# Performance work log

Hardware: AMD Instinct MI355X
Metric: run time of the kernel (lower is better)

## Reference

```python
import jax, jax.numpy as jnp
import numpy as np

N, H = 8192, 1024

def setup_inputs() -> dict:
    key = jax.random.key(0)
    ks = jax.random.split(key, 7)
    s = 1.0 / np.sqrt(H)
    return {
        "x": jax.random.normal(ks[0], (N, H), dtype=jnp.float32),
        "Wq": jax.random.uniform(ks[1], (H, H), dtype=jnp.float32, minval=-s, maxval=s),
        "bq": jax.random.uniform(ks[2], (H,), dtype=jnp.float32, minval=-s, maxval=s),
        "Wk": jax.random.uniform(ks[3], (H, H), dtype=jnp.float32, minval=-s, maxval=s),
        "bk": jax.random.uniform(ks[4], (H,), dtype=jnp.float32, minval=-s, maxval=s),
        "Wv": jax.random.uniform(ks[5], (H, H), dtype=jnp.float32, minval=-s, maxval=s),
        "bv": jax.random.uniform(ks[6], (H,), dtype=jnp.float32, minval=-s, maxval=s),
    }

def reference(x, Wq, bq, Wk, bk, Wv, bv):
    # q/k/v projections: [N, H]
    q = x @ Wq + bq
    k = x @ Wk + bk
    v = x @ Wv + bv
    # full scores [N, N]; NOTE: original has no 1/sqrt(d) scaling
    scores = q @ k.T
    alpha = jax.nn.softmax(scores, axis=1)
    return alpha @ v
```

## Files before the change

kernel.cpp:

```cpp
#include <hip/hip_runtime.h>
#include <hip/hip_bf16.h>
#include <hip/hip_fp16.h>


typedef _Float16 f16x8 __attribute__((ext_vector_type(8)));
typedef _Float16 f16x2 __attribute__((ext_vector_type(2)));
typedef float floatx4 __attribute__((ext_vector_type(4)));
typedef float floatx2 __attribute__((ext_vector_type(2)));

__device__ __forceinline__ unsigned short f2h(float f) {
  __half h = __float2half(f);
  return __builtin_bit_cast(unsigned short, h);
}
__device__ __forceinline__ float h2f(unsigned short u) {
  return __half2float(__builtin_bit_cast(__half, u));
}

__device__ __forceinline__ float fdot2(unsigned a, unsigned b, float c) {
#if __has_builtin(__builtin_amdgcn_fdot2)
  return __builtin_amdgcn_fdot2(__builtin_bit_cast(f16x2, a),
                                __builtin_bit_cast(f16x2, b), c, false);
#else
  f16x2 av = __builtin_bit_cast(f16x2, a);
  f16x2 bv = __builtin_bit_cast(f16x2, b);
  return c + (float)av[0] * (float)bv[0] + (float)av[1] * (float)bv[1];
#endif
}

__device__ __forceinline__ void async16(const void* g, void* l) {
  __builtin_amdgcn_global_load_lds(
      (__attribute__((address_space(1))) unsigned int*)(g),
      (__attribute__((address_space(3))) unsigned int*)(l),
      16, 0, 0);
}


__global__ __launch_bounds__(256) void conv_f32_f16(const float* __restrict__ in,
                                                    unsigned short* __restrict__ out,
                                                    long n) {
  long i = ((long)blockIdx.x * 256 + threadIdx.x) * 4;
  if (i + 3 < n) {
    float4 f = *(const float4*)(in + i);
    ushort4 o;
    o.x = f2h(f.x); o.y = f2h(f.y); o.z = f2h(f.z); o.w = f2h(f.w);
    *(ushort4*)(out + i) = o;
  }
}

__global__ __launch_bounds__(256) void transpose_f32_f16_3(const float* __restrict__ in0,
                                                           const float* __restrict__ in1,
                                                           const float* __restrict__ in2,
                                                           unsigned short* __restrict__ out,
                                                           int rows, int cols) {
  const float* in = (blockIdx.z == 0) ? in0 : (blockIdx.z == 1) ? in1 : in2;
  unsigned short* o = out + (size_t)blockIdx.z * rows * cols;
  __shared__ float tile[32][33];
  int bx = blockIdx.x * 32;
  int by = blockIdx.y * 32;
  int tx = threadIdx.x & 31, ty = threadIdx.x >> 5;
  #pragma unroll
  for (int yy = ty; yy < 32; yy += 8)
    tile[yy][tx] = in[(size_t)(by + yy) * cols + bx + tx];
  __syncthreads();
  #pragma unroll
  for (int yy = ty; yy < 32; yy += 8)
    o[(size_t)(bx + yy) * rows + by + tx] = f2h(tile[tx][yy]);
}

template <int MODE>
__global__ __launch_bounds__(256, 4)
void gemm_bt(const unsigned short* __restrict__ A,
             const unsigned short* __restrict__ B,
             int M, int Nn, int K,
             const float* __restrict__ b0, const float* __restrict__ b1,
             const float* __restrict__ b2,
             unsigned short* __restrict__ out) {
  if constexpr (MODE == 0) {
    B   += (size_t)blockIdx.z * Nn * K;
    out += (size_t)blockIdx.z * M * Nn;
  }
  const float* bias = (MODE != 0) ? nullptr
                      : (blockIdx.z == 0) ? b0 : (blockIdx.z == 1) ? b1 : b2;

  unsigned bx = blockIdx.x, by = blockIdx.y;
  if constexpr (MODE == 1) {
    const unsigned nb  = gridDim.x * gridDim.y;
    const unsigned lin = blockIdx.y * gridDim.x + blockIdx.x;
    const unsigned swz = (lin & 7u) * (nb >> 3) + (lin >> 3);
    bx = swz % gridDim.x;
    by = swz / gridDim.x;
  }

  __shared__ unsigned short As[128 * 32];
  __shared__ unsigned short Bs[128 * 32];
  const int tid  = threadIdx.x;
  const int wave = tid >> 6;
  const int lane = tid & 63;
  const int wm = wave >> 1, wn = wave & 1;
  const int quad = lane >> 4, l16 = lane & 15;
  const long bm = (long)by * 128;
  const long bn = (long)bx * 128;

  floatx4 acc[4][4] = {};

  const int srow = wave * 32 + (lane >> 2);
  const int scol = (lane & 3) * 8;
  const unsigned short* gA0 = A + (bm + srow) * (long)K + scol;
  const unsigned short* gA1 = gA0 + 16L * K;
  const unsigned short* gB0 = B + (bn + srow) * (long)K + scol;
  const unsigned short* gB1 = gB0 + 16L * K;
  unsigned short* lA0 = &As[(wave * 32) * 32];
  unsigned short* lA1 = &As[(wave * 32 + 16) * 32];
  unsigned short* lB0 = &Bs[(wave * 32) * 32];
  unsigned short* lB1 = &Bs[(wave * 32 + 16) * 32];

  for (int kk = 0; kk < K; kk += 32) {
    async16(gA0 + kk, lA0);
    async16(gA1 + kk, lA1);
    async16(gB0 + kk, lB0);
    async16(gB1 + kk, lB1);
    __syncthreads();
    f16x8 af[4], bfv[4];
    #pragma unroll
    for (int i = 0; i < 4; ++i) {
      af[i]  = *reinterpret_cast<const f16x8*>(&As[(wm * 64 + i * 16 + l16) * 32 + quad * 8]);
      bfv[i] = *reinterpret_cast<const f16x8*>(&Bs[(wn * 64 + i * 16 + l16) * 32 + quad * 8]);
    }
    #pragma unroll
    for (int i = 0; i < 4; ++i)
      #pragma unroll
      for (int j = 0; j < 4; ++j)
        acc[i][j] = __builtin_amdgcn_mfma_f32_16x16x32_f16(af[i], bfv[j], acc[i][j], 0, 0, 0);
    __syncthreads();
  }

  #pragma unroll
  for (int i = 0; i < 4; ++i) {
    const long row0 = bm + wm * 64 + i * 16 + quad * 4;
    #pragma unroll
    for (int j = 0; j < 4; ++j) {
      const long col = bn + wn * 64 + j * 16 + l16;
      const float cb = (MODE == 0) ? bias[col] : 0.0f;
      #pragma unroll
      for (int r = 0; r < 4; ++r)
        out[(row0 + r) * (long)Nn + col] = f2h(acc[i][j][r] + cb);
    }
  }
}

__global__ __launch_bounds__(256) void softmax_compact(unsigned short* __restrict__ S,
                                                       int* __restrict__ nnz, int n) {
  const int row = blockIdx.x;
  const int tid = threadIdx.x;
  const int lane = tid & 63, w = tid >> 6;
  unsigned short* prow = S + (size_t)row * n;
  const __half* hrow = (const __half*)prow;

  float v[32];
  float m = -1e30f;
  #pragma unroll
  for (int i = 0; i < 32; ++i) {
    v[i] = __half2float(hrow[i * 256 + tid]);
    m = fmaxf(m, v[i]);
  }
  #pragma unroll
  for (int off = 32; off > 0; off >>= 1) m = fmaxf(m, __shfl_down(m, off, 64));
  __shared__ float redm[4];
  __shared__ int cnt;
  if (lane == 0) redm[w] = m;
  if (tid == 0) cnt = 0;
  __syncthreads();
  m = fmaxf(fmaxf(redm[0], redm[1]), fmaxf(redm[2], redm[3]));

  float s = 0.0f;
  #pragma unroll
  for (int i = 0; i < 32; ++i) {
    v[i] = __expf(v[i] - m);
    s += v[i];
  }
  #pragma unroll
  for (int off = 32; off > 0; off >>= 1) s += __shfl_down(s, off, 64);
  __shared__ float reds[4];
  if (lane == 0) reds[w] = s;
  __syncthreads();
  s = reds[0] + reds[1] + reds[2] + reds[3];
  const float inv = 1.0f / s;

  unsigned int* pairs = (unsigned int*)prow;
  const int cap = n / 2;
  #pragma unroll
  for (int i = 0; i < 32; ++i) {
    unsigned short hh = f2h(v[i] * inv);
    if (hh) {
      int p = atomicAdd(&cnt, 1);
      if (p < cap) pairs[p] = ((unsigned int)(i * 256 + tid) << 16) | hh;
    }
  }
  __syncthreads();
  const int c = (cnt < cap) ? cnt : cap;
  const int padded = (c + 7) & ~7;
  if (tid < padded - c) pairs[c + tid] = 0u;
  if (tid == 0) nnz[row] = padded;
}

__global__ __launch_bounds__(256) void pv_sliced(const unsigned short* __restrict__ S,
                                                 const int* __restrict__ nnz,
                                                 const unsigned short* __restrict__ v,
                                                 float* __restrict__ out,
                                                 int n) {
  const int wave = threadIdx.x >> 6;
  const int lane = threadIdx.x & 63;
  const int colbase = blockIdx.x * 128 + lane * 2;
  const unsigned colbyte = (unsigned)colbase * 2;
  const char* __restrict__ vb = (const char*)v;
  const char* __restrict__ sb = (const char*)S;

#define GOFF(p) ((((p) >> 16) << 11) + colbyte)
#define GLD(p) (*(const unsigned*)(vb + GOFF(p)))
#define MATH2(pa, pb, ga, gb)                                                  \
  {                                                                            \
    const unsigned w01 = __builtin_amdgcn_perm(pb, pa, 0x05040100u);           \
    a0 = fdot2(w01, __builtin_amdgcn_perm(gb, ga, 0x05040100u), a0);           \
    a1 = fdot2(w01, __builtin_amdgcn_perm(gb, ga, 0x07060302u), a1);           \
  }

  #pragma unroll 1
  for (int r = 0; r < 8; ++r) {
    const int row = blockIdx.y + ((wave << 3) + r) * 256;
    int craw = nnz[row];
    craw = craw < 0 ? 0 : (craw > 4096 ? 4096 : craw);
    const int cnt = __builtin_amdgcn_readfirstlane(craw);
    float a0 = 0.f, a1 = 0.f;
    if (cnt > 0) {
      const unsigned rowbase = (unsigned)row << 14;
      const unsigned plast = rowbase + (unsigned)(cnt - 8) * 4;
      uint4 c0 = *(const uint4*)(sb + rowbase);
      uint4 c1 = *(const uint4*)(sb + rowbase + 16);
      unsigned g0 = GLD(c0.x), g1 = GLD(c0.y), g2 = GLD(c0.z), g3 = GLD(c0.w);
      unsigned g4 = GLD(c1.x), g5 = GLD(c1.y), g6 = GLD(c1.z), g7 = GLD(c1.w);
      unsigned pn = rowbase + 32 <= plast ? rowbase + 32 : plast;
      uint4 n0 = *(const uint4*)(sb + pn);
      uint4 n1 = *(const uint4*)(sb + pn + 16);
      for (int j = 0; j < cnt; j += 8) {
        const unsigned h0 = GLD(n0.x), h1 = GLD(n0.y), h2 = GLD(n0.z), h3 = GLD(n0.w);
        const unsigned h4 = GLD(n1.x), h5 = GLD(n1.y), h6 = GLD(n1.z), h7 = GLD(n1.w);
        const unsigned pn2 = pn + 32 <= plast ? pn + 32 : plast;
        const uint4 m0 = *(const uint4*)(sb + pn2);
        const uint4 m1 = *(const uint4*)(sb + pn2 + 16);
        MATH2(c0.x, c0.y, g0, g1)
        MATH2(c0.z, c0.w, g2, g3)
        MATH2(c1.x, c1.y, g4, g5)
        MATH2(c1.z, c1.w, g6, g7)
        c0 = n0; c1 = n1;
        g0 = h0; g1 = h1; g2 = h2; g3 = h3;
        g4 = h4; g5 = h5; g6 = h6; g7 = h7;
        n0 = m0; n1 = m1; pn = pn2;
      }
    }
    floatx2 o = {a0, a1};
    __builtin_nontemporal_store(o, (floatx2*)(out + ((size_t)row << 10) + colbase));
  }
#undef MATH2
#undef GLD
#undef GOFF
}

extern "C" void kernel_launch(void* const* d_in, const int* in_sizes, int n_in,
                              void* d_out, int out_size, void* d_ws, size_t ws_size,
                              hipStream_t stream) {
  const int N = 8192, H = 1024;
  const float* x  = (const float*)d_in[0];
  const float* Wq = (const float*)d_in[1];
  const float* bq = (const float*)d_in[2];
  const float* Wk = (const float*)d_in[3];
  const float* bk = (const float*)d_in[4];
  const float* Wv = (const float*)d_in[5];
  const float* bv = (const float*)d_in[6];

  char* p = (char*)d_ws;
  unsigned short* xh  = (unsigned short*)p; p += (size_t)N * H * 2;
  unsigned short* WT  = (unsigned short*)p; p += (size_t)3 * H * H * 2;
  unsigned short* qkv = (unsigned short*)p; p += (size_t)3 * N * H * 2;
  unsigned short* S   = (unsigned short*)p; p += (size_t)N * N * 2;
  int*            nnz = (int*)p;            p += (size_t)N * 4;
  if ((size_t)(p - (char*)d_ws) > ws_size) return;
  unsigned short* qh = qkv;
  unsigned short* kh = qkv + (size_t)N * H;
  unsigned short* vh = qkv + (size_t)2 * N * H;

  conv_f32_f16<<<(N * H / 4 + 255) / 256, 256, 0, stream>>>(x, xh, (long)N * H);
  transpose_f32_f16_3<<<dim3(H / 32, H / 32, 3), 256, 0, stream>>>(Wq, Wk, Wv, WT, H, H);

  gemm_bt<0><<<dim3(H / 128, N / 128, 3), 256, 0, stream>>>(xh, WT, N, H, H,
                                                            bq, bk, bv, qkv);

  gemm_bt<1><<<dim3(N / 128, N / 128), 256, 0, stream>>>(qh, kh, N, N, H,
                                                         nullptr, nullptr, nullptr, S);
  softmax_compact<<<N, 256, 0, stream>>>(S, nnz, N);
  pv_sliced<<<dim3(8, N / 32), 256, 0, stream>>>(S, nnz, vh, (float*)d_out, N);
}
```

Baseline: 560.1 us.

## Interleave two sparse softmax rows per wave in PV gather loop

The sparse PV kernel now processes two rows at once per wave, interleaving their gathers and dot products so twice as many independent loads are in flight to hide gather latency. Shorter rows pad to the longer row's iteration count by reading a zeroed 8-entry tail, which the softmax compaction kernel now writes. The score GEMM in MODE 1 uses nontemporal stores for its output. The change raises register pressure and spends wasted iterations when two rows have very different nonzero counts.

```diff
diff --git a/kernel.cpp b/kernel.cpp
--- a/kernel.cpp
+++ b/kernel.cpp
@@ -142,8 +142,13 @@
       const long col = bn + wn * 64 + j * 16 + l16;
       const float cb = (MODE == 0) ? bias[col] : 0.0f;
       #pragma unroll
-      for (int r = 0; r < 4; ++r)
-        out[(row0 + r) * (long)Nn + col] = f2h(acc[i][j][r] + cb);
+      for (int r = 0; r < 4; ++r) {
+        const unsigned short hv = f2h(acc[i][j][r] + cb);
+        if constexpr (MODE == 1)
+          __builtin_nontemporal_store(hv, &out[(row0 + r) * (long)Nn + col]);
+        else
+          out[(row0 + r) * (long)Nn + col] = hv;
+      }
     }
   }
 }
@@ -200,6 +205,8 @@
   const int c = (cnt < cap) ? cnt : cap;
   const int padded = (c + 7) & ~7;
   if (tid < padded - c) pairs[c + tid] = 0u;
+  const int zq = (padded <= cap - 8) ? padded : cap - 8;
+  if (tid < 8) pairs[zq + tid] = 0u;
   if (tid == 0) nnz[row] = padded;
 }
 
@@ -217,48 +224,76 @@
 
 #define GOFF(p) ((((p) >> 16) << 11) + colbyte)
 #define GLD(p) (*(const unsigned*)(vb + GOFF(p)))
-#define MATH2(pa, pb, ga, gb)                                                  \
+#define MATH2(pa, pb, ga, gb, A0, A1)                                          \
   {                                                                            \
     const unsigned w01 = __builtin_amdgcn_perm(pb, pa, 0x05040100u);           \
-    a0 = fdot2(w01, __builtin_amdgcn_perm(gb, ga, 0x05040100u), a0);           \
-    a1 = fdot2(w01, __builtin_amdgcn_perm(gb, ga, 0x07060302u), a1);           \
+    A0 = fdot2(w01, __builtin_amdgcn_perm(gb, ga, 0x05040100u), A0);           \
+    A1 = fdot2(w01, __builtin_amdgcn_perm(gb, ga, 0x07060302u), A1);           \
   }
 
   #pragma unroll 1
-  for (int r = 0; r < 8; ++r) {
-    const int row = blockIdx.y + ((wave << 3) + r) * 256;
-    int craw = nnz[row];
-    craw = craw < 0 ? 0 : (craw > 4096 ? 4096 : craw);
-    const int cnt = __builtin_amdgcn_readfirstlane(craw);
-    float a0 = 0.f, a1 = 0.f;
-    if (cnt > 0) {
-      const unsigned rowbase = (unsigned)row << 14;
-      const unsigned plast = rowbase + (unsigned)(cnt - 8) * 4;
-      uint4 c0 = *(const uint4*)(sb + rowbase);
-      uint4 c1 = *(const uint4*)(sb + rowbase + 16);
-      unsigned g0 = GLD(c0.x), g1 = GLD(c0.y), g2 = GLD(c0.z), g3 = GLD(c0.w);
-      unsigned g4 = GLD(c1.x), g5 = GLD(c1.y), g6 = GLD(c1.z), g7 = GLD(c1.w);
-      unsigned pn = rowbase + 32 <= plast ? rowbase + 32 : plast;
-      uint4 n0 = *(const uint4*)(sb + pn);
-      uint4 n1 = *(const uint4*)(sb + pn + 16);
-      for (int j = 0; j < cnt; j += 8) {
-        const unsigned h0 = GLD(n0.x), h1 = GLD(n0.y), h2 = GLD(n0.z), h3 = GLD(n0.w);
-        const unsigned h4 = GLD(n1.x), h5 = GLD(n1.y), h6 = GLD(n1.z), h7 = GLD(n1.w);
-        const unsigned pn2 = pn + 32 <= plast ? pn + 32 : plast;
-        const uint4 m0 = *(const uint4*)(sb + pn2);
-        const uint4 m1 = *(const uint4*)(sb + pn2 + 16);
-        MATH2(c0.x, c0.y, g0, g1)
-        MATH2(c0.z, c0.w, g2, g3)
-        MATH2(c1.x, c1.y, g4, g5)
-        MATH2(c1.z, c1.w, g6, g7)
-        c0 = n0; c1 = n1;
-        g0 = h0; g1 = h1; g2 = h2; g3 = h3;
-        g4 = h4; g5 = h5; g6 = h6; g7 = h7;
-        n0 = m0; n1 = m1; pn = pn2;
-      }
+  for (int rp = 0; rp < 4; ++rp) {
+    const int rowA = blockIdx.y + ((wave << 3) + rp * 2) * 256;
+    const int rowB = rowA + 256;
+    int ra = nnz[rowA]; ra = ra < 8 ? 8 : (ra > 4096 ? 4096 : ra);
+    int rb = nnz[rowB]; rb = rb < 8 ? 8 : (rb > 4096 ? 4096 : rb);
+    const int cA = __builtin_amdgcn_readfirstlane(ra);
+    const int cB = __builtin_amdgcn_readfirstlane(rb);
+    const unsigned baseA = (unsigned)rowA << 14;
+    const unsigned baseB = (unsigned)rowB << 14;
+    const unsigned lastA = baseA + (unsigned)(cA - 8) * 4;
+    const unsigned lastB = baseB + (unsigned)(cB - 8) * 4;
+    const unsigned zqA = baseA + (unsigned)(cA <= 4088 ? cA : 4088) * 4;
+    const unsigned zqB = baseB + (unsigned)(cB <= 4088 ? cB : 4088) * 4;
+
+    uint4 cA0 = *(const uint4*)(sb + baseA);
+    uint4 cA1 = *(const uint4*)(sb + baseA + 16);
+    uint4 cB0 = *(const uint4*)(sb + baseB);
+    uint4 cB1 = *(const uint4*)(sb + baseB + 16);
+    unsigned gA0 = GLD(cA0.x), gA1 = GLD(cA0.y), gA2 = GLD(cA0.z), gA3 = GLD(cA0.w);
+    unsigned gA4 = GLD(cA1.x), gA5 = GLD(cA1.y), gA6 = GLD(cA1.z), gA7 = GLD(cA1.w);
+    unsigned gB0 = GLD(cB0.x), gB1 = GLD(cB0.y), gB2 = GLD(cB0.z), gB3 = GLD(cB0.w);
+    unsigned gB4 = GLD(cB1.x), gB5 = GLD(cB1.y), gB6 = GLD(cB1.z), gB7 = GLD(cB1.w);
+    unsigned pA = (baseA + 32 <= lastA) ? baseA + 32 : zqA;
+    unsigned pB = (baseB + 32 <= lastB) ? baseB + 32 : zqB;
+    uint4 nA0 = *(const uint4*)(sb + pA);
+    uint4 nA1 = *(const uint4*)(sb + pA + 16);
+    uint4 nB0 = *(const uint4*)(sb + pB);
+    uint4 nB1 = *(const uint4*)(sb + pB + 16);
+
+    float aA0 = 0.f, aA1 = 0.f, aB0 = 0.f, aB1 = 0.f;
+    const int itn = (cA > cB ? cA : cB) >> 3;
+    for (int t = 0; t < itn; ++t) {
+      const unsigned hA0 = GLD(nA0.x), hA1 = GLD(nA0.y), hA2 = GLD(nA0.z), hA3 = GLD(nA0.w);
+      const unsigned hA4 = GLD(nA1.x), hA5 = GLD(nA1.y), hA6 = GLD(nA1.z), hA7 = GLD(nA1.w);
+      const unsigned hB0 = GLD(nB0.x), hB1 = GLD(nB0.y), hB2 = GLD(nB0.z), hB3 = GLD(nB0.w);
+      const unsigned hB4 = GLD(nB1.x), hB5 = GLD(nB1.y), hB6 = GLD(nB1.z), hB7 = GLD(nB1.w);
+      const unsigned qA = (pA + 32 <= lastA) ? pA + 32 : zqA;
+      const unsigned qB = (pB + 32 <= lastB) ? pB + 32 : zqB;
+      const uint4 mA0 = *(const uint4*)(sb + qA);
+      const uint4 mA1 = *(const uint4*)(sb + qA + 16);
+      const uint4 mB0 = *(const uint4*)(sb + qB);
+      const uint4 mB1 = *(const uint4*)(sb + qB + 16);
+      MATH2(cA0.x, cA0.y, gA0, gA1, aA0, aA1)
+      MATH2(cA0.z, cA0.w, gA2, gA3, aA0, aA1)
+      MATH2(cA1.x, cA1.y, gA4, gA5, aA0, aA1)
+      MATH2(cA1.z, cA1.w, gA6, gA7, aA0, aA1)
+      MATH2(cB0.x, cB0.y, gB0, gB1, aB0, aB1)
+      MATH2(cB0.z, cB0.w, gB2, gB3, aB0, aB1)
+      MATH2(cB1.x, cB1.y, gB4, gB5, aB0, aB1)
+      MATH2(cB1.z, cB1.w, gB6, gB7, aB0, aB1)
+      cA0 = nA0; cA1 = nA1; cB0 = nB0; cB1 = nB1;
+      gA0 = hA0; gA1 = hA1; gA2 = hA2; gA3 = hA3;
+      gA4 = hA4; gA5 = hA5; gA6 = hA6; gA7 = hA7;
+      gB0 = hB0; gB1 = hB1; gB2 = hB2; gB3 = hB3;
+      gB4 = hB4; gB5 = hB5; gB6 = hB6; gB7 = hB7;
+      nA0 = mA0; nA1 = mA1; nB0 = mB0; nB1 = mB1;
+      pA = qA; pB = qB;
     }
-    floatx2 o = {a0, a1};
-    __builtin_nontemporal_store(o, (floatx2*)(out + ((size_t)row << 10) + colbase));
+    floatx2 oA = {aA0, aA1};
+    floatx2 oB = {aB0, aB1};
+    __builtin_nontemporal_store(oA, (floatx2*)(out + ((size_t)rowA << 10) + colbase));
+    __builtin_nontemporal_store(oB, (floatx2*)(out + ((size_t)rowB << 10) + colbase));
   }
 #undef MATH2
 #undef GLD
```

New measurement: 636.3 us. 13.6% more time.
